# Kernel optimization log

Measured on AMD Instinct MI355X. Metric: run time of the kernel, lower is better.

The kernel has to match this reference:

```python
import jax, jax.numpy as jnp
import numpy as np

N = 50000      # nodes
E = 1_600_000  # edges
D = 512        # input_dim == embedding_dim (see notes: fc_emb output is dead code)
H = 256        # hidden_channels
G = 16         # graphs in the batch


def setup_inputs() -> dict:
    key = jax.random.key(0)
    ks = jax.random.split(key, 16)
    x = jax.random.normal(ks[0], (N, D), dtype=jnp.float32)
    edge_index = jax.random.randint(ks[1], (2, E), 0, N, dtype=jnp.int64)
    batch = jnp.sort(jax.random.randint(ks[2], (N,), 0, G, dtype=jnp.int64))

    def lin(k, fi, fo):
        s = 1.0 / np.sqrt(fi)
        return jax.random.uniform(k, (fi, fo), jnp.float32, -s, s)

    return {
        "x": x,
        "edge_index": edge_index,
        "batch": batch,
        "W1": lin(ks[3], D, H), "b1": jnp.zeros((H,), jnp.float32),
        "W2": lin(ks[4], H, H), "b2": jnp.zeros((H,), jnp.float32),
        "W3": lin(ks[5], H, H), "b3": jnp.zeros((H,), jnp.float32),
        "Wf": lin(ks[6], H, 64), "bf": jnp.zeros((64,), jnp.float32),
        "Wp": lin(ks[7], 64, 1), "bp": jnp.zeros((1,), jnp.float32),
    }


def _gcn_conv(h, src, dst, norm, W, b):
    # GCNConv: out[i] = sum_{j->i} norm_ji * (h[j] @ W) + b  (self-loops included in src/dst)
    m = h @ W                                    # [N, out]  transform first (smaller gather)
    agg = jax.ops.segment_sum(m[src] * norm[:, None], dst, num_segments=N)
    return agg + b


def reference(x, edge_index, batch, W1, b1, W2, b2, W3, b3, Wf, bf, Wp, bp):
    loops = jnp.arange(N, dtype=edge_index.dtype)
    src = jnp.concatenate([edge_index[0], loops])   # [E+N]
    dst = jnp.concatenate([edge_index[1], loops])
    # symmetric normalization D^{-1/2} (A+I) D^{-1/2}; degree over targets incl. self-loops
    deg = jax.ops.segment_sum(jnp.ones_like(dst, jnp.float32), dst, num_segments=N)
    dinv = jnp.where(deg > 0, jax.lax.rsqrt(deg), 0.0)
    norm = dinv[src] * dinv[dst]                    # [E+N]

    h = jax.nn.relu(_gcn_conv(x, src, dst, norm, W1, b1))
    h = jax.nn.relu(_gcn_conv(h, src, dst, norm, W2, b2))
    h = _gcn_conv(h, src, dst, norm, W3, b3)

    # global_mean_pool over graph ids
    counts = jax.ops.segment_sum(jnp.ones((N,), jnp.float32), batch, num_segments=G)
    pooled = jax.ops.segment_sum(h, batch, num_segments=G) / jnp.maximum(counts, 1.0)[:, None]

    # dropout treated as identity (eval-mode determinism for baseline)
    out = pooled @ Wf + bf
    out = out @ Wp + bp
    return jax.nn.sigmoid(out)
```

## Files before the change

### kernel.cpp

```cpp
#include <hip/hip_runtime.h>
#include <hip/hip_bf16.h>

#define NN 50000
#define EE 1600000
#define DD 512
#define HH 256
#define GG 16
#define BK 96
#define NCH 256
#define CHSZ 6250

typedef long fp8x8;
typedef __attribute__((ext_vector_type(4))) float f32x4;
typedef __attribute__((ext_vector_type(2))) float f32x2;

__device__ __forceinline__ unsigned char f2fp8(float f) {
    return (unsigned char)(__builtin_amdgcn_cvt_pk_fp8_f32(f, f, 0, false) & 0xff);
}
__device__ __forceinline__ unsigned int pk4fp8(float a, float b, float c, float d) {
    unsigned int r = __builtin_amdgcn_cvt_pk_fp8_f32(a, b, 0, false);
    return __builtin_amdgcn_cvt_pk_fp8_f32(c, d, r, true);
}

__global__ __launch_bounds__(256) void k_hist_cvt(const int* __restrict__ ei,
                                                  unsigned int* __restrict__ histg,
                                                  const float* __restrict__ x, unsigned char* __restrict__ xb,
                                                  const float* __restrict__ W1, const float* __restrict__ W2,
                                                  const float* __restrict__ W3, unsigned char* __restrict__ W1t,
                                                  unsigned char* __restrict__ W2t, unsigned char* __restrict__ W3t) {
    __shared__ unsigned int hp[6250];
    int b = blockIdx.x, t = threadIdx.x;
    if (b < 512) {
        int j = b >> 1, half = b & 1;
        int dlo = half * 25000;
        for (int i = t; i < 6250; i += 256) hp[i] = 0;
        __syncthreads();
        int base = j * CHSZ;
        for (int k = 0; k < 25; ++k) {
            int o = k * 256 + t;
            if (o < CHSZ) {
                int d = ei[EE + base + o];
                unsigned int ld = (unsigned)(d - dlo);
                if (ld < 25000u) atomicAdd(&hp[ld >> 2], 1u << ((ld & 3) * 8));
            }
        }
        __syncthreads();
        unsigned int* dst = histg + (size_t)j * 12500 + half * 6250;
        for (int i = t; i < 6250; i += 256) dst[i] = hp[i];
    } else if (b < 6762) {
        size_t i0 = ((size_t)(b - 512) * 256 + t) * 16;
        float4 v0 = *(const float4*)(x + i0);
        float4 v1 = *(const float4*)(x + i0 + 4);
        float4 v2 = *(const float4*)(x + i0 + 8);
        float4 v3 = *(const float4*)(x + i0 + 12);
        uint4 o;
        o.x = pk4fp8(v0.x, v0.y, v0.z, v0.w);
        o.y = pk4fp8(v1.x, v1.y, v1.z, v1.w);
        o.z = pk4fp8(v2.x, v2.y, v2.z, v2.w);
        o.w = pk4fp8(v3.x, v3.y, v3.z, v3.w);
        *(uint4*)(xb + i0) = o;
    } else {
        int u = (b - 6762) * 256 + t;
        if (u < 131072) {
            int k = u >> 8, n = u & 255;
            W1t[(size_t)n * 512 + k] = f2fp8(W1[u]);
        } else if (u < 196608) {
            int q = u - 131072; int k = q >> 8, n = q & 255;
            W2t[(size_t)n * 256 + k] = f2fp8(W2[q]);
        } else {
            int q = u - 196608; int k = q >> 8, n = q & 255;
            W3t[(size_t)n * 256 + k] = f2fp8(W3[q]);
        }
    }
}

__global__ __launch_bounds__(256) void k_scan(const unsigned int* __restrict__ histg,
                                              unsigned int* __restrict__ offg,
                                              int* __restrict__ cnt, float* __restrict__ dinv,
                                              unsigned int* __restrict__ zero0) {
    __shared__ unsigned int part[512];
    int t = threadIdx.x, b = blockIdx.x;
    if (b == 391) {
        for (int i = t; i < GG * 256 + GG + 1; i += 256) zero0[i] = 0u;
        return;
    }
    const int il = t & 31, g = t >> 5;
    const int g4 = b * 32 + il;
    const bool ok = (g4 < 12500);
    unsigned hv[32];
    unsigned s02 = 0, s13 = 0;
    if (ok) {
        const unsigned* hp = histg + (size_t)(g * 32) * 12500 + g4;
        #pragma unroll
        for (int jj = 0; jj < 32; ++jj) hv[jj] = hp[(size_t)jj * 12500];
        #pragma unroll
        for (int jj = 0; jj < 32; ++jj) { s02 += hv[jj] & 0x00ff00ffu; s13 += (hv[jj] >> 8) & 0x00ff00ffu; }
    }
    part[t * 2] = s02; part[t * 2 + 1] = s13;
    __syncthreads();
    unsigned b02 = 0, b13 = 0;
    #pragma unroll
    for (int g2 = 0; g2 < 7; ++g2)
        if (g2 < g) { b02 += part[(g2 * 32 + il) * 2]; b13 += part[(g2 * 32 + il) * 2 + 1]; }
    if (ok && g == 7) {
        unsigned t02 = b02 + s02, t13 = b13 + s13;
        int4 cv; cv.x = (int)(t02 & 0xffffu); cv.y = (int)(t13 & 0xffffu);
        cv.z = (int)(t02 >> 16);      cv.w = (int)(t13 >> 16);
        *(int4*)(cnt + 4 * g4) = cv;
        float4 dv;
        dv.x = rsqrtf((float)cv.x + 1.0f); dv.y = rsqrtf((float)cv.y + 1.0f);
        dv.z = rsqrtf((float)cv.z + 1.0f); dv.w = rsqrtf((float)cv.w + 1.0f);
        *(float4*)(dinv + 4 * g4) = dv;
    }
    if (ok) {
        unsigned r0 = b02 & 0xffffu, r2 = b02 >> 16, r1 = b13 & 0xffffu, r3 = b13 >> 16;
        #pragma unroll
        for (int jj = 0; jj < 32; ++jj) {
            uint2 wv; wv.x = r0 | (r1 << 16); wv.y = r2 | (r3 << 16);
            *(uint2*)(offg + (size_t)(g * 32 + jj) * 25000 + 2 * g4) = wv;
            unsigned h = hv[jj];
            r0 += h & 0xffu; r1 += (h >> 8) & 0xffu; r2 += (h >> 16) & 0xffu; r3 += h >> 24;
        }
    }
}

__global__ __launch_bounds__(256) void k_place(const int* __restrict__ ei,
                                               const unsigned int* __restrict__ offg,
                                               unsigned short* __restrict__ bucket) {
    __shared__ unsigned int cur[3125];
    int b = blockIdx.x, t = threadIdx.x;
    int x8 = b & 7, j = b >> 3;
    int lo = x8 * CHSZ;
    for (int i = t; i < 3125; i += 256) cur[i] = 0;
    __syncthreads();
    int base = j * CHSZ;
    for (int k = 0; k < 25; ++k) {
        int o = k * 256 + t;
        if (o < CHSZ) {
            int d = ei[EE + base + o];
            unsigned ld = (unsigned)(d - lo);
            if (ld < 6250u) {
                int s = ei[base + o];
                unsigned old = atomicAdd(&cur[ld >> 1], (ld & 1) ? 65536u : 1u);
                unsigned rank = (ld & 1) ? (old >> 16) : (old & 0xffffu);
                unsigned ov = offg[j * 25000 + (d >> 1)];
                unsigned pos = ((d & 1) ? (ov >> 16) : (ov & 0xffffu)) + rank;
                if (pos < BK) bucket[(size_t)d * BK + pos] = (unsigned short)s;
            }
        }
    }
}

__global__ __launch_bounds__(256) void k_sort(const int* __restrict__ cnt,
                                              const unsigned short* __restrict__ bucket,
                                              unsigned short* __restrict__ bucket2) {
    __shared__ unsigned int binc[4][16], rk[4][16];
    int w = threadIdx.x >> 6, l = threadIdx.x & 63;
    int node = blockIdx.x * 4 + w;
    if (l < 16) { binc[w][l] = 0; rk[w][l] = 0; }
    __syncthreads();
    int n = cnt[node]; if (n > BK) n = BK;
    const unsigned short* cs = bucket + (size_t)node * BK;
    unsigned s0 = 0, s1 = 0; int b0 = -1, b1 = -1;
    if (l < n)      { s0 = cs[l];      b0 = (int)(s0 >> 12); atomicAdd(&binc[w][b0], 1u); }
    if (l + 64 < n) { s1 = cs[l + 64]; b1 = (int)(s1 >> 12); atomicAdd(&binc[w][b1], 1u); }
    __syncthreads();
    unsigned short* ds = bucket2 + (size_t)node * BK;
    if (b0 >= 0) {
        unsigned base = 0;
        for (int q = 0; q < b0; ++q) base += binc[w][q];
        ds[base + atomicAdd(&rk[w][b0], 1u)] = (unsigned short)s0;
    }
    if (b1 >= 0) {
        unsigned base = 0;
        for (int q = 0; q < b1; ++q) base += binc[w][q];
        ds[base + atomicAdd(&rk[w][b1], 1u)] = (unsigned short)s1;
    }
}

__global__ __launch_bounds__(256) void k_gemm_fp8(const unsigned char* __restrict__ A,
                                                  const unsigned char* __restrict__ Bt,
                                                  const float* __restrict__ dinv,
                                                  unsigned char* __restrict__ C, int M, int K) {
    __shared__ unsigned char As[2][8192];
    __shared__ unsigned char Bs[2][8192];
    const int tid  = threadIdx.x;
    const int wave = tid >> 6;
    const int lane = tid & 63;
    const int row0 = blockIdx.x * 128;
    const int col0 = blockIdx.y * 128;
    const int wr = wave & 1;
    const int wc = wave >> 1;
    const int l15 = lane & 15;
    const int quad = lane >> 4;

    const int srow = (wave << 4) + (lane >> 2);
    const int gk16 = (((lane & 3) ^ (srow & 3)) << 4);
    int arow1 = row0 + srow;      if (arow1 >= M) arow1 = M - 1;
    int arow2 = row0 + srow + 64; if (arow2 >= M) arow2 = M - 1;
    const int brow1 = col0 + srow;
    const int brow2 = brow1 + 64;

#define STAGE(BUF, KB) do {                                                              \
    const unsigned char* ga1_ = A  + (size_t)arow1 * K + (KB) + gk16;                    \
    const unsigned char* ga2_ = A  + (size_t)arow2 * K + (KB) + gk16;                    \
    const unsigned char* gb1_ = Bt + (size_t)brow1 * K + (KB) + gk16;                    \
    const unsigned char* gb2_ = Bt + (size_t)brow2 * K + (KB) + gk16;                    \
    __builtin_amdgcn_global_load_lds((const __attribute__((address_space(1))) void*)ga1_,\
        (__attribute__((address_space(3))) void*)&As[BUF][wave * 1024], 16, 0, 0);       \
    __builtin_amdgcn_global_load_lds((const __attribute__((address_space(1))) void*)ga2_,\
        (__attribute__((address_space(3))) void*)&As[BUF][4096 + wave * 1024], 16, 0, 0);\
    __builtin_amdgcn_global_load_lds((const __attribute__((address_space(1))) void*)gb1_,\
        (__attribute__((address_space(3))) void*)&Bs[BUF][wave * 1024], 16, 0, 0);       \
    __builtin_amdgcn_global_load_lds((const __attribute__((address_space(1))) void*)gb2_,\
        (__attribute__((address_space(3))) void*)&Bs[BUF][4096 + wave * 1024], 16, 0, 0);\
} while (0)

    f32x4 acc[4][4];
    #pragma unroll
    for (int i = 0; i < 4; ++i)
        #pragma unroll
        for (int j = 0; j < 4; ++j)
            acc[i][j] = (f32x4){0.f, 0.f, 0.f, 0.f};

    const int NT = K >> 6;
    STAGE(0, 0);
    __syncthreads();

    for (int t = 0; t < NT; ++t) {
        const int cb = t & 1;
        if (t + 1 < NT) STAGE(cb ^ 1, (t + 1) << 6);

        fp8x8 af[2][4], bfr[2][4];
        #pragma unroll
        for (int kk = 0; kk < 2; ++kk) {
            const int csw = (((kk * 2 + (quad >> 1)) ^ (l15 & 3)) << 4) + ((quad & 1) << 3);
            #pragma unroll
            for (int mi = 0; mi < 4; ++mi) {
                af[kk][mi]  = *(const fp8x8*)&As[cb][(wr * 64 + mi * 16 + l15) * 64 + csw];
                bfr[kk][mi] = *(const fp8x8*)&Bs[cb][(wc * 64 + mi * 16 + l15) * 64 + csw];
            }
        }
        #pragma unroll
        for (int kk = 0; kk < 2; ++kk)
            #pragma unroll
            for (int mi = 0; mi < 4; ++mi)
                #pragma unroll
                for (int ni = 0; ni < 4; ++ni)
                    acc[mi][ni] = __builtin_amdgcn_mfma_f32_16x16x32_fp8_fp8(af[kk][mi], bfr[kk][ni], acc[mi][ni], 0, 0, 0);

        __syncthreads();
    }
#undef STAGE

    #pragma unroll
    for (int mi = 0; mi < 4; ++mi) {
        #pragma unroll
        for (int r = 0; r < 4; ++r) {
            int grow = row0 + wr * 64 + mi * 16 + quad * 4 + r;
            if (grow < M) {
                float ds = dinv[grow];
                #pragma unroll
                for (int ni = 0; ni < 4; ++ni) {
                    int gcol = col0 + wc * 64 + ni * 16 + l15;
                    C[(size_t)grow * 256 + gcol] = f2fp8(ds * acc[mi][ni][r]);
                }
            }
        }
    }
}

__global__ __launch_bounds__(256) void k_agg(const unsigned int* __restrict__ m,
                                             const float* __restrict__ bias,
                                             const float* __restrict__ dinv, const int* __restrict__ cnt,
                                             const unsigned short* __restrict__ bucket,
                                             unsigned int* __restrict__ outb,
                                             int do_relu) {
    int lane = threadIdx.x & 63;
    int node = blockIdx.x * 4 + (threadIdx.x >> 6);
    if (node >= NN) return;
    const unsigned int* mrow = m + lane;
    unsigned int v = mrow[(size_t)node * 64];
    f32x2 lo = __builtin_amdgcn_cvt_pk_f32_fp8(v, false);
    f32x2 hi = __builtin_amdgcn_cvt_pk_f32_fp8(v, true);
    float4 acc = make_float4(lo.x, lo.y, hi.x, hi.y);
    int n = cnt[node]; if (n > BK) n = BK;
    const unsigned short* cs = bucket + (size_t)node * BK;
    int p = 0;
    for (; p + 16 <= n; p += 16) {
        uint4 iv0 = *(const uint4*)(cs + p);
        uint4 iv1 = *(const uint4*)(cs + p + 8);
        unsigned int u0 = mrow[(size_t)(iv0.x & 0xffffu) * 64];
        unsigned int u1 = mrow[(size_t)(iv0.x >> 16)    * 64];
        unsigned int u2 = mrow[(size_t)(iv0.y & 0xffffu) * 64];
        unsigned int u3 = mrow[(size_t)(iv0.y >> 16)    * 64];
        unsigned int u4 = mrow[(size_t)(iv0.z & 0xffffu) * 64];
        unsigned int u5 = mrow[(size_t)(iv0.z >> 16)    * 64];
        unsigned int u6 = mrow[(size_t)(iv0.w & 0xffffu) * 64];
        unsigned int u7 = mrow[(size_t)(iv0.w >> 16)    * 64];
        unsigned int u8 = mrow[(size_t)(iv1.x & 0xffffu) * 64];
        unsigned int u9 = mrow[(size_t)(iv1.x >> 16)    * 64];
        unsigned int ua = mrow[(size_t)(iv1.y & 0xffffu) * 64];
        unsigned int ub = mrow[(size_t)(iv1.y >> 16)    * 64];
        unsigned int uc = mrow[(size_t)(iv1.z & 0xffffu) * 64];
        unsigned int ud = mrow[(size_t)(iv1.z >> 16)    * 64];
        unsigned int ue = mrow[(size_t)(iv1.w & 0xffffu) * 64];
        unsigned int uf = mrow[(size_t)(iv1.w >> 16)    * 64];
        f32x2 a0 = __builtin_amdgcn_cvt_pk_f32_fp8(u0, false), b0 = __builtin_amdgcn_cvt_pk_f32_fp8(u0, true);
        f32x2 a1 = __builtin_amdgcn_cvt_pk_f32_fp8(u1, false), b1 = __builtin_amdgcn_cvt_pk_f32_fp8(u1, true);
        f32x2 a2 = __builtin_amdgcn_cvt_pk_f32_fp8(u2, false), b2 = __builtin_amdgcn_cvt_pk_f32_fp8(u2, true);
        f32x2 a3 = __builtin_amdgcn_cvt_pk_f32_fp8(u3, false), b3 = __builtin_amdgcn_cvt_pk_f32_fp8(u3, true);
        f32x2 a4 = __builtin_amdgcn_cvt_pk_f32_fp8(u4, false), b4 = __builtin_amdgcn_cvt_pk_f32_fp8(u4, true);
        f32x2 a5 = __builtin_amdgcn_cvt_pk_f32_fp8(u5, false), b5 = __builtin_amdgcn_cvt_pk_f32_fp8(u5, true);
        f32x2 a6 = __builtin_amdgcn_cvt_pk_f32_fp8(u6, false), b6 = __builtin_amdgcn_cvt_pk_f32_fp8(u6, true);
        f32x2 a7 = __builtin_amdgcn_cvt_pk_f32_fp8(u7, false), b7 = __builtin_amdgcn_cvt_pk_f32_fp8(u7, true);
        f32x2 a8 = __builtin_amdgcn_cvt_pk_f32_fp8(u8, false), b8 = __builtin_amdgcn_cvt_pk_f32_fp8(u8, true);
        f32x2 a9 = __builtin_amdgcn_cvt_pk_f32_fp8(u9, false), b9 = __builtin_amdgcn_cvt_pk_f32_fp8(u9, true);
        f32x2 aa = __builtin_amdgcn_cvt_pk_f32_fp8(ua, false), ba = __builtin_amdgcn_cvt_pk_f32_fp8(ua, true);
        f32x2 ab = __builtin_amdgcn_cvt_pk_f32_fp8(ub, false), bb2 = __builtin_amdgcn_cvt_pk_f32_fp8(ub, true);
        f32x2 ac = __builtin_amdgcn_cvt_pk_f32_fp8(uc, false), bc = __builtin_amdgcn_cvt_pk_f32_fp8(uc, true);
        f32x2 ad = __builtin_amdgcn_cvt_pk_f32_fp8(ud, false), bd = __builtin_amdgcn_cvt_pk_f32_fp8(ud, true);
        f32x2 ae = __builtin_amdgcn_cvt_pk_f32_fp8(ue, false), be = __builtin_amdgcn_cvt_pk_f32_fp8(ue, true);
        f32x2 af2 = __builtin_amdgcn_cvt_pk_f32_fp8(uf, false), bf2 = __builtin_amdgcn_cvt_pk_f32_fp8(uf, true);
        acc.x += (((a0.x + a1.x) + (a2.x + a3.x)) + ((a4.x + a5.x) + (a6.x + a7.x)))
               + (((a8.x + a9.x) + (aa.x + ab.x)) + ((ac.x + ad.x) + (ae.x + af2.x)));
        acc.y += (((a0.y + a1.y) + (a2.y + a3.y)) + ((a4.y + a5.y) + (a6.y + a7.y)))
               + (((a8.y + a9.y) + (aa.y + ab.y)) + ((ac.y + ad.y) + (ae.y + af2.y)));
        acc.z += (((b0.x + b1.x) + (b2.x + b3.x)) + ((b4.x + b5.x) + (b6.x + b7.x)))
               + (((b8.x + b9.x) + (ba.x + bb2.x)) + ((bc.x + bd.x) + (be.x + bf2.x)));
        acc.w += (((b0.y + b1.y) + (b2.y + b3.y)) + ((b4.y + b5.y) + (b6.y + b7.y)))
               + (((b8.y + b9.y) + (ba.y + bb2.y)) + ((bc.y + bd.y) + (be.y + bf2.y)));
    }
    for (; p + 8 <= n; p += 8) {
        uint4 iv0 = *(const uint4*)(cs + p);
        unsigned int u0 = mrow[(size_t)(iv0.x & 0xffffu) * 64];
        unsigned int u1 = mrow[(size_t)(iv0.x >> 16)    * 64];
        unsigned int u2 = mrow[(size_t)(iv0.y & 0xffffu) * 64];
        unsigned int u3 = mrow[(size_t)(iv0.y >> 16)    * 64];
        unsigned int u4 = mrow[(size_t)(iv0.z & 0xffffu) * 64];
        unsigned int u5 = mrow[(size_t)(iv0.z >> 16)    * 64];
        unsigned int u6 = mrow[(size_t)(iv0.w & 0xffffu) * 64];
        unsigned int u7 = mrow[(size_t)(iv0.w >> 16)    * 64];
        f32x2 a0 = __builtin_amdgcn_cvt_pk_f32_fp8(u0, false), b0 = __builtin_amdgcn_cvt_pk_f32_fp8(u0, true);
        f32x2 a1 = __builtin_amdgcn_cvt_pk_f32_fp8(u1, false), b1 = __builtin_amdgcn_cvt_pk_f32_fp8(u1, true);
        f32x2 a2 = __builtin_amdgcn_cvt_pk_f32_fp8(u2, false), b2 = __builtin_amdgcn_cvt_pk_f32_fp8(u2, true);
        f32x2 a3 = __builtin_amdgcn_cvt_pk_f32_fp8(u3, false), b3 = __builtin_amdgcn_cvt_pk_f32_fp8(u3, true);
        f32x2 a4 = __builtin_amdgcn_cvt_pk_f32_fp8(u4, false), b4 = __builtin_amdgcn_cvt_pk_f32_fp8(u4, true);
        f32x2 a5 = __builtin_amdgcn_cvt_pk_f32_fp8(u5, false), b5 = __builtin_amdgcn_cvt_pk_f32_fp8(u5, true);
        f32x2 a6 = __builtin_amdgcn_cvt_pk_f32_fp8(u6, false), b6 = __builtin_amdgcn_cvt_pk_f32_fp8(u6, true);
        f32x2 a7 = __builtin_amdgcn_cvt_pk_f32_fp8(u7, false), b7 = __builtin_amdgcn_cvt_pk_f32_fp8(u7, true);
        acc.x += ((a0.x + a1.x) + (a2.x + a3.x)) + ((a4.x + a5.x) + (a6.x + a7.x));
        acc.y += ((a0.y + a1.y) + (a2.y + a3.y)) + ((a4.y + a5.y) + (a6.y + a7.y));
        acc.z += ((b0.x + b1.x) + (b2.x + b3.x)) + ((b4.x + b5.x) + (b6.x + b7.x));
        acc.w += ((b0.y + b1.y) + (b2.y + b3.y)) + ((b4.y + b5.y) + (b6.y + b7.y));
    }
    for (; p < n; ++p) {
        int s = cs[p];
        unsigned int u = mrow[(size_t)s * 64];
        f32x2 a = __builtin_amdgcn_cvt_pk_f32_fp8(u, false);
        f32x2 b = __builtin_amdgcn_cvt_pk_f32_fp8(u, true);
        acc.x += a.x; acc.y += a.y; acc.z += b.x; acc.w += b.y;
    }
    float di = dinv[node];
    const float4 bb = *(const float4*)(bias + lane * 4);
    acc.x = acc.x * di + bb.x; acc.y = acc.y * di + bb.y;
    acc.z = acc.z * di + bb.z; acc.w = acc.w * di + bb.w;
    if (do_relu) {
        acc.x = fmaxf(acc.x, 0.f); acc.y = fmaxf(acc.y, 0.f);
        acc.z = fmaxf(acc.z, 0.f); acc.w = fmaxf(acc.w, 0.f);
    }
    outb[(size_t)node * 64 + lane] = pk4fp8(acc.x, acc.y, acc.z, acc.w);
}

__global__ __launch_bounds__(256) void k_poolhead(const unsigned int* __restrict__ h,
                                                  const int* __restrict__ batch,
                                                  float* __restrict__ pooled, float* __restrict__ cnts,
                                                  unsigned int* __restrict__ ctr,
                                                  const float* __restrict__ Wf, const float* __restrict__ bf,
                                                  const float* __restrict__ Wp, const float* __restrict__ bp,
                                                  float* __restrict__ out) {
    __shared__ float pl[GG * 256];
    __shared__ float cl[GG];
    __shared__ float z[GG][64];
    __shared__ unsigned int lastdone;
    int t = threadIdx.x;
    for (int i = t; i < GG * 256; i += 256) pl[i] = 0.f;
    if (t < GG) cl[t] = 0.f;
    __syncthreads();
    int sub = t >> 6;
    int fd = t & 63;
    int chunk = (NN + gridDim.x - 1) / gridDim.x;
    int i0 = blockIdx.x * chunk;
    int i1 = i0 + chunk; if (i1 > NN) i1 = NN;
    int gcur = -1;
    float a0 = 0.f, a1 = 0.f, a2 = 0.f, a3 = 0.f, cr = 0.f;
    for (int i = i0 + sub; i < i1; i += 4) {
        int g = batch[i];
        if (g != gcur) {
            if (gcur >= 0) {
                atomicAdd(&pl[gcur * 256 + fd * 4 + 0], a0);
                atomicAdd(&pl[gcur * 256 + fd * 4 + 1], a1);
                atomicAdd(&pl[gcur * 256 + fd * 4 + 2], a2);
                atomicAdd(&pl[gcur * 256 + fd * 4 + 3], a3);
                if (fd == 0) atomicAdd(&cl[gcur], cr);
            }
            gcur = g; a0 = a1 = a2 = a3 = 0.f; cr = 0.f;
        }
        unsigned int u = h[(size_t)i * 64 + fd];
        f32x2 lo = __builtin_amdgcn_cvt_pk_f32_fp8(u, false);
        f32x2 hi = __builtin_amdgcn_cvt_pk_f32_fp8(u, true);
        a0 += lo.x; a1 += lo.y; a2 += hi.x; a3 += hi.y;
        cr += 1.f;
    }
    if (gcur >= 0) {
        atomicAdd(&pl[gcur * 256 + fd * 4 + 0], a0);
        atomicAdd(&pl[gcur * 256 + fd * 4 + 1], a1);
        atomicAdd(&pl[gcur * 256 + fd * 4 + 2], a2);
        atomicAdd(&pl[gcur * 256 + fd * 4 + 3], a3);
        if (fd == 0) atomicAdd(&cl[gcur], cr);
    }
    __syncthreads();
    for (int i = t; i < GG * 256; i += 256)
        if (pl[i] != 0.f) atomicAdd(&pooled[i], pl[i]);
    if (t < GG && cl[t] != 0.f) atomicAdd(&cnts[t], cl[t]);

    __syncthreads();
    __threadfence();
    if (t == 0) lastdone = (atomicAdd(ctr, 1u) == gridDim.x - 1) ? 1u : 0u;
    __syncthreads();
    if (!lastdone) return;
    __threadfence();
    for (int i = t; i < GG * 256; i += 256)
        pl[i] = __hip_atomic_load(&pooled[i], __ATOMIC_RELAXED, __HIP_MEMORY_SCOPE_AGENT);
    if (t < GG)
        cl[t] = __hip_atomic_load(&cnts[t], __ATOMIC_RELAXED, __HIP_MEMORY_SCOPE_AGENT);
    __syncthreads();
    for (int idx = t; idx < GG * 64; idx += 256) {
        int g = idx >> 6, j = idx & 63;
        float inv = 1.f / fmaxf(cl[g], 1.f);
        float acc = 0.f;
        for (int k = 0; k < 256; ++k) acc += pl[g * 256 + k] * Wf[k * 64 + j];
        z[g][j] = acc * inv + bf[j];
    }
    __syncthreads();
    if (t < GG) {
        float o = 0.f;
        for (int j2 = 0; j2 < 64; ++j2) o += z[t][j2] * Wp[j2];
        o += bp[0];
        out[t] = 1.f / (1.f + expf(-o));
    }
}

extern "C" void kernel_launch(void* const* d_in, const int* in_sizes, int n_in,
                              void* d_out, int out_size, void* d_ws, size_t ws_size,
                              hipStream_t stream) {
    const float* x   = (const float*)d_in[0];
    const int*   ei  = (const int*)d_in[1];
    const int*   bat = (const int*)d_in[2];
    const float* W1  = (const float*)d_in[3];
    const float* b1  = (const float*)d_in[4];
    const float* W2  = (const float*)d_in[5];
    const float* b2  = (const float*)d_in[6];
    const float* W3  = (const float*)d_in[7];
    const float* b3  = (const float*)d_in[8];
    const float* Wf  = (const float*)d_in[9];
    const float* bf  = (const float*)d_in[10];
    const float* Wp  = (const float*)d_in[11];
    const float* bp  = (const float*)d_in[12];
    float* out = (float*)d_out;

    char* w = (char*)d_ws;
    unsigned char* xb  = (unsigned char*)w;  w += (size_t)NN * DD;
    unsigned char* mb  = (unsigned char*)w;  w += (size_t)NN * HH;
    unsigned char* hb  = (unsigned char*)w;  w += (size_t)NCH * 25000 * 4;
    unsigned char* hb2 = (unsigned char*)w;  w += (size_t)NCH * 25000 * 4;
    unsigned char* W1t = (unsigned char*)w;  w += (size_t)DD * HH;
    unsigned char* W2t = (unsigned char*)w;  w += (size_t)HH * HH;
    unsigned char* W3t = (unsigned char*)w;  w += (size_t)HH * HH;
    float* dinv   = (float*)w;               w += (size_t)NN * 4;
    int*   cnt    = (int*)w;                 w += (size_t)NN * 4;
    unsigned short* bucket  = (unsigned short*)w; w += (size_t)NN * BK * 2;
    unsigned short* bucket2 = (unsigned short*)w; w += (size_t)NN * BK * 2;
    float* pooled = (float*)w;               w += (size_t)GG * HH * 4;
    float* cnts   = (float*)w;               w += (size_t)GG * 4;
    unsigned int* ctr = (unsigned int*)w;    w += 4;

    unsigned int* histg = (unsigned int*)hb;
    unsigned int* offg  = (unsigned int*)hb2;

    k_hist_cvt<<<7786, 256, 0, stream>>>(ei, histg, x, xb, W1, W2, W3, W1t, W2t, W3t);
    k_scan<<<392, 256, 0, stream>>>(histg, offg, cnt, dinv, (unsigned int*)pooled);
    k_place<<<2048, 256, 0, stream>>>(ei, offg, bucket);
    k_sort<<<12500, 256, 0, stream>>>(cnt, bucket, bucket2);

    dim3 gg((NN + 127) / 128, 2);
    k_gemm_fp8<<<gg, 256, 0, stream>>>(xb, W1t, dinv, mb, NN, DD);
    k_agg<<<(NN + 3) / 4, 256, 0, stream>>>((const unsigned int*)mb, b1, dinv, cnt, bucket2,
                                            (unsigned int*)hb, 1);
    k_gemm_fp8<<<gg, 256, 0, stream>>>(hb, W2t, dinv, mb, NN, HH);
    k_agg<<<(NN + 3) / 4, 256, 0, stream>>>((const unsigned int*)mb, b2, dinv, cnt, bucket2,
                                            (unsigned int*)hb2, 1);
    k_gemm_fp8<<<gg, 256, 0, stream>>>(hb2, W3t, dinv, mb, NN, HH);
    k_agg<<<(NN + 3) / 4, 256, 0, stream>>>((const unsigned int*)mb, b3, dinv, cnt, bucket2,
                                            (unsigned int*)hb, 0);

    k_poolhead<<<256, 256, 0, stream>>>((const unsigned int*)hb, bat, pooled, cnts, ctr,
                                        Wf, bf, Wp, bp, out);
}
```

Measured before the change: 545.8 us.

## Drop per-node source sort pass and compute graph counts via binary search

Removes the k_sort kernel that reordered each node's neighbour list by source block, so aggregation now reads the unsorted bucket directly. This saves a launch and a pass over the bucket array, at the cost of less local gather order in k_agg. Pooling now uses 2000 blocks of 25 nodes each, and the last block gets per-graph node counts by binary searching the sorted batch array instead of accumulating them with atomics. The counts buffer and its zeroing are removed.

After: 627.2 us. 14.9% more time.

```diff
diff --git a/kernel.cpp b/kernel.cpp
--- a/kernel.cpp
+++ b/kernel.cpp
@@ -81,7 +81,7 @@
     __shared__ unsigned int part[512];
     int t = threadIdx.x, b = blockIdx.x;
     if (b == 391) {
-        for (int i = t; i < GG * 256 + GG + 1; i += 256) zero0[i] = 0u;
+        for (int i = t; i < GG * 256 + 1; i += 256) zero0[i] = 0u;
         return;
     }
     const int il = t & 31, g = t >> 5;
@@ -148,33 +148,6 @@
                 if (pos < BK) bucket[(size_t)d * BK + pos] = (unsigned short)s;
             }
         }
-    }
-}
-
-__global__ __launch_bounds__(256) void k_sort(const int* __restrict__ cnt,
-                                              const unsigned short* __restrict__ bucket,
-                                              unsigned short* __restrict__ bucket2) {
-    __shared__ unsigned int binc[4][16], rk[4][16];
-    int w = threadIdx.x >> 6, l = threadIdx.x & 63;
-    int node = blockIdx.x * 4 + w;
-    if (l < 16) { binc[w][l] = 0; rk[w][l] = 0; }
-    __syncthreads();
-    int n = cnt[node]; if (n > BK) n = BK;
-    const unsigned short* cs = bucket + (size_t)node * BK;
-    unsigned s0 = 0, s1 = 0; int b0 = -1, b1 = -1;
-    if (l < n)      { s0 = cs[l];      b0 = (int)(s0 >> 12); atomicAdd(&binc[w][b0], 1u); }
-    if (l + 64 < n) { s1 = cs[l + 64]; b1 = (int)(s1 >> 12); atomicAdd(&binc[w][b1], 1u); }
-    __syncthreads();
-    unsigned short* ds = bucket2 + (size_t)node * BK;
-    if (b0 >= 0) {
-        unsigned base = 0;
-        for (int q = 0; q < b0; ++q) base += binc[w][q];
-        ds[base + atomicAdd(&rk[w][b0], 1u)] = (unsigned short)s0;
-    }
-    if (b1 >= 0) {
-        unsigned base = 0;
-        for (int q = 0; q < b1; ++q) base += binc[w][q];
-        ds[base + atomicAdd(&rk[w][b1], 1u)] = (unsigned short)s1;
     }
 }
 
@@ -374,26 +347,25 @@
 
 __global__ __launch_bounds__(256) void k_poolhead(const unsigned int* __restrict__ h,
                                                   const int* __restrict__ batch,
-                                                  float* __restrict__ pooled, float* __restrict__ cnts,
+                                                  float* __restrict__ pooled,
                                                   unsigned int* __restrict__ ctr,
                                                   const float* __restrict__ Wf, const float* __restrict__ bf,
                                                   const float* __restrict__ Wp, const float* __restrict__ bp,
                                                   float* __restrict__ out) {
     __shared__ float pl[GG * 256];
+    __shared__ float z[GG][64];
+    __shared__ unsigned int ub[GG];
     __shared__ float cl[GG];
-    __shared__ float z[GG][64];
     __shared__ unsigned int lastdone;
     int t = threadIdx.x;
     for (int i = t; i < GG * 256; i += 256) pl[i] = 0.f;
-    if (t < GG) cl[t] = 0.f;
     __syncthreads();
     int sub = t >> 6;
     int fd = t & 63;
-    int chunk = (NN + gridDim.x - 1) / gridDim.x;
-    int i0 = blockIdx.x * chunk;
-    int i1 = i0 + chunk; if (i1 > NN) i1 = NN;
+    int i0 = blockIdx.x * 25;
+    int i1 = i0 + 25;
     int gcur = -1;
-    float a0 = 0.f, a1 = 0.f, a2 = 0.f, a3 = 0.f, cr = 0.f;
+    float a0 = 0.f, a1 = 0.f, a2 = 0.f, a3 = 0.f;
     for (int i = i0 + sub; i < i1; i += 4) {
         int g = batch[i];
         if (g != gcur) {
@@ -402,27 +374,23 @@
                 atomicAdd(&pl[gcur * 256 + fd * 4 + 1], a1);
                 atomicAdd(&pl[gcur * 256 + fd * 4 + 2], a2);
                 atomicAdd(&pl[gcur * 256 + fd * 4 + 3], a3);
-                if (fd == 0) atomicAdd(&cl[gcur], cr);
             }
-            gcur = g; a0 = a1 = a2 = a3 = 0.f; cr = 0.f;
+            gcur = g; a0 = a1 = a2 = a3 = 0.f;
         }
         unsigned int u = h[(size_t)i * 64 + fd];
         f32x2 lo = __builtin_amdgcn_cvt_pk_f32_fp8(u, false);
         f32x2 hi = __builtin_amdgcn_cvt_pk_f32_fp8(u, true);
         a0 += lo.x; a1 += lo.y; a2 += hi.x; a3 += hi.y;
-        cr += 1.f;
     }
     if (gcur >= 0) {
         atomicAdd(&pl[gcur * 256 + fd * 4 + 0], a0);
         atomicAdd(&pl[gcur * 256 + fd * 4 + 1], a1);
         atomicAdd(&pl[gcur * 256 + fd * 4 + 2], a2);
         atomicAdd(&pl[gcur * 256 + fd * 4 + 3], a3);
-        if (fd == 0) atomicAdd(&cl[gcur], cr);
     }
     __syncthreads();
     for (int i = t; i < GG * 256; i += 256)
         if (pl[i] != 0.f) atomicAdd(&pooled[i], pl[i]);
-    if (t < GG && cl[t] != 0.f) atomicAdd(&cnts[t], cl[t]);
 
     __syncthreads();
     __threadfence();
@@ -432,8 +400,13 @@
     __threadfence();
     for (int i = t; i < GG * 256; i += 256)
         pl[i] = __hip_atomic_load(&pooled[i], __ATOMIC_RELAXED, __HIP_MEMORY_SCOPE_AGENT);
-    if (t < GG)
-        cl[t] = __hip_atomic_load(&cnts[t], __ATOMIC_RELAXED, __HIP_MEMORY_SCOPE_AGENT);
+    if (t < GG) {
+        int lo2 = 0, hi2 = NN;
+        while (lo2 < hi2) { int mid = (lo2 + hi2) >> 1; if (batch[mid] <= t) lo2 = mid + 1; else hi2 = mid; }
+        ub[t] = (unsigned)lo2;
+    }
+    __syncthreads();
+    if (t < GG) cl[t] = (float)(ub[t] - (t ? ub[t - 1] : 0u));
     __syncthreads();
     for (int idx = t; idx < GG * 64; idx += 256) {
         int g = idx >> 6, j = idx & 63;
@@ -479,10 +452,8 @@
     unsigned char* W3t = (unsigned char*)w;  w += (size_t)HH * HH;
     float* dinv   = (float*)w;               w += (size_t)NN * 4;
     int*   cnt    = (int*)w;                 w += (size_t)NN * 4;
-    unsigned short* bucket  = (unsigned short*)w; w += (size_t)NN * BK * 2;
-    unsigned short* bucket2 = (unsigned short*)w; w += (size_t)NN * BK * 2;
+    unsigned short* bucket = (unsigned short*)w; w += (size_t)NN * BK * 2;
     float* pooled = (float*)w;               w += (size_t)GG * HH * 4;
-    float* cnts   = (float*)w;               w += (size_t)GG * 4;
     unsigned int* ctr = (unsigned int*)w;    w += 4;
 
     unsigned int* histg = (unsigned int*)hb;
@@ -491,19 +462,18 @@
     k_hist_cvt<<<7786, 256, 0, stream>>>(ei, histg, x, xb, W1, W2, W3, W1t, W2t, W3t);
     k_scan<<<392, 256, 0, stream>>>(histg, offg, cnt, dinv, (unsigned int*)pooled);
     k_place<<<2048, 256, 0, stream>>>(ei, offg, bucket);
-    k_sort<<<12500, 256, 0, stream>>>(cnt, bucket, bucket2);
 
     dim3 gg((NN + 127) / 128, 2);
     k_gemm_fp8<<<gg, 256, 0, stream>>>(xb, W1t, dinv, mb, NN, DD);
-    k_agg<<<(NN + 3) / 4, 256, 0, stream>>>((const unsigned int*)mb, b1, dinv, cnt, bucket2,
+    k_agg<<<(NN + 3) / 4, 256, 0, stream>>>((const unsigned int*)mb, b1, dinv, cnt, bucket,
                                             (unsigned int*)hb, 1);
     k_gemm_fp8<<<gg, 256, 0, stream>>>(hb, W2t, dinv, mb, NN, HH);
-    k_agg<<<(NN + 3) / 4, 256, 0, stream>>>((const unsigned int*)mb, b2, dinv, cnt, bucket2,
+    k_agg<<<(NN + 3) / 4, 256, 0, stream>>>((const unsigned int*)mb, b2, dinv, cnt, bucket,
                                             (unsigned int*)hb2, 1);
     k_gemm_fp8<<<gg, 256, 0, stream>>>(hb2, W3t, dinv, mb, NN, HH);
-    k_agg<<<(NN + 3) / 4, 256, 0, stream>>>((const unsigned int*)mb, b3, dinv, cnt, bucket2,
+    k_agg<<<(NN + 3) / 4, 256, 0, stream>>>((const unsigned int*)mb, b3, dinv, cnt, bucket,
                                             (unsigned int*)hb, 0);
 
-    k_poolhead<<<256, 256, 0, stream>>>((const unsigned int*)hb, bat, pooled, cnts, ctr,
-                                        Wf, bf, Wp, bp, out);
-}
+    k_poolhead<<<2000, 256, 0, stream>>>((const unsigned int*)hb, bat, pooled, ctr,
+                                         Wf, bf, Wp, bp, out);
+}
```
